# Optimization experiments

Measured on AMD Instinct MI355X. Metric: run time of the kernel, lower is better.

Reference implementation:

```python
import jax, jax.numpy as jnp
import numpy as np

B, N, C = 8192, 4, 4096
SINKHORN_ITERS = 3
EPS = 1e-6


def setup_inputs() -> dict:
    key = jax.random.key(0)
    k_x, k_w, k_pre, k_post, k_res = jax.random.split(key, 5)
    x = jax.random.normal(k_x, (B, N, C), dtype=jnp.float32)
    # Parameters (torch inits: weight=ones, H_pre/H_post=zeros, H_res=eye);
    # use small random perturbations so gradients/normalizations are nontrivial.
    rmsnorm_weight = jnp.ones((C,), jnp.float32) + 0.01 * jax.random.normal(k_w, (C,), jnp.float32)
    H_pre = 0.1 * jax.random.normal(k_pre, (N,), jnp.float32)
    H_post = 0.1 * jax.random.normal(k_post, (N,), jnp.float32)
    H_res = jnp.eye(N, dtype=jnp.float32) + 0.1 * jax.random.normal(k_res, (N, N), jnp.float32)
    return {"x": x, "rmsnorm_weight": rmsnorm_weight, "H_pre": H_pre, "H_post": H_post, "H_res": H_res}


def reference(x, rmsnorm_weight, H_pre, H_post, H_res):
    xf = x.astype(jnp.float32)                                  # [B, n, C]
    # stream aggregation with sigmoid-gated pre-weights
    H_pre_act = jax.nn.sigmoid(H_pre)                           # [n]
    x_agg = jnp.einsum('bnc,n->bc', xf, H_pre_act)              # [B, C]
    # bf16 round-trip mirrors the torch .to(bfloat16) cast before RMSNorm
    x_agg_bf = x_agg.astype(jnp.bfloat16).astype(jnp.float32)
    rms = jnp.sqrt(jnp.mean(x_agg_bf ** 2, axis=-1, keepdims=True) + EPS)  # [B, 1]
    y_norm = x_agg_bf / rms * rmsnorm_weight[None, :]           # [B, C]
    # Sinkhorn-Knopp: doubly-stochastic projection of exp(H_res), n x n (tiny)
    P = jnp.exp(H_res)
    for _ in range(SINKHORN_ITERS):
        P = P / (jnp.sum(P, axis=-1, keepdims=True) + EPS)
        P = P / (jnp.sum(P, axis=-2, keepdims=True) + EPS)
    H_post_act = 2.0 * jax.nn.sigmoid(H_post)                   # [n]
    mixed = jnp.einsum('ij,bjc->bic', P, xf)                    # [B, n, C]
    return mixed + H_post_act[None, :, None] * y_norm[:, None, :]
```

## Files before the change

kernel.cpp:

```cpp
#include <hip/hip_runtime.h>
#include <hip/hip_bf16.h>


constexpr int Bb = 8192;
constexpr int Nn = 4;
constexpr int Cc = 4096;
constexpr int THREADS = 256;
constexpr int C4 = Cc / 4;
constexpr int VPT = C4 / THREADS;

__global__ __launch_bounds__(THREADS)
void mhc_kernel(const float* __restrict__ x,
                const float* __restrict__ w,
                const float* __restrict__ H_pre,
                const float* __restrict__ H_post,
                const float* __restrict__ H_res,
                float* __restrict__ out)
{
    const int b = blockIdx.x;
    const int t = threadIdx.x;

    float pre[4], post[4], P[4][4];
#pragma unroll
    for (int n = 0; n < 4; ++n) {
        pre[n]  = 1.0f / (1.0f + expf(-H_pre[n]));
        post[n] = 2.0f / (1.0f + expf(-H_post[n]));
    }
#pragma unroll
    for (int i = 0; i < 4; ++i)
#pragma unroll
        for (int j = 0; j < 4; ++j)
            P[i][j] = expf(H_res[i * 4 + j]);
#pragma unroll
    for (int it = 0; it < 3; ++it) {
#pragma unroll
        for (int i = 0; i < 4; ++i) {
            float s = P[i][0] + P[i][1] + P[i][2] + P[i][3] + 1e-6f;
            float r = 1.0f / s;
#pragma unroll
            for (int j = 0; j < 4; ++j) P[i][j] *= r;
        }
#pragma unroll
        for (int j = 0; j < 4; ++j) {
            float s = P[0][j] + P[1][j] + P[2][j] + P[3][j] + 1e-6f;
            float r = 1.0f / s;
#pragma unroll
            for (int i = 0; i < 4; ++i) P[i][j] *= r;
        }
    }

    const float4* xb = (const float4*)(x + (size_t)b * Nn * Cc);
    float4 xv[4][VPT];
#pragma unroll
    for (int n = 0; n < 4; ++n)
#pragma unroll
        for (int v = 0; v < VPT; ++v)
            xv[n][v] = xb[n * C4 + v * THREADS + t];

    float4 aggbf[VPT];
    float ssq = 0.0f;
#pragma unroll
    for (int v = 0; v < VPT; ++v) {
        float4 a;
        a.x = pre[0]*xv[0][v].x + pre[1]*xv[1][v].x + pre[2]*xv[2][v].x + pre[3]*xv[3][v].x;
        a.y = pre[0]*xv[0][v].y + pre[1]*xv[1][v].y + pre[2]*xv[2][v].y + pre[3]*xv[3][v].y;
        a.z = pre[0]*xv[0][v].z + pre[1]*xv[1][v].z + pre[2]*xv[2][v].z + pre[3]*xv[3][v].z;
        a.w = pre[0]*xv[0][v].w + pre[1]*xv[1][v].w + pre[2]*xv[2][v].w + pre[3]*xv[3][v].w;
        a.x = __bfloat162float(__float2bfloat16(a.x));
        a.y = __bfloat162float(__float2bfloat16(a.y));
        a.z = __bfloat162float(__float2bfloat16(a.z));
        a.w = __bfloat162float(__float2bfloat16(a.w));
        ssq += a.x*a.x + a.y*a.y + a.z*a.z + a.w*a.w;
        aggbf[v] = a;
    }

#pragma unroll
    for (int off = 32; off > 0; off >>= 1)
        ssq += __shfl_down(ssq, off, 64);
    __shared__ float wsum[4];
    const int wid  = t >> 6;
    const int lane = t & 63;
    if (lane == 0) wsum[wid] = ssq;
    __syncthreads();
    const float tot = wsum[0] + wsum[1] + wsum[2] + wsum[3];
    const float rms_inv = 1.0f / sqrtf(tot * (1.0f / (float)Cc) + 1e-6f);

    const float4* w4 = (const float4*)w;
    float4* ob = (float4*)(out + (size_t)b * Nn * Cc);
#pragma unroll
    for (int v = 0; v < VPT; ++v) {
        const int idx = v * THREADS + t;
        const float4 wv = w4[idx];
        float4 yn;
        yn.x = aggbf[v].x * rms_inv * wv.x;
        yn.y = aggbf[v].y * rms_inv * wv.y;
        yn.z = aggbf[v].z * rms_inv * wv.z;
        yn.w = aggbf[v].w * rms_inv * wv.w;
#pragma unroll
        for (int i = 0; i < 4; ++i) {
            float4 o;
            o.x = P[i][0]*xv[0][v].x + P[i][1]*xv[1][v].x + P[i][2]*xv[2][v].x + P[i][3]*xv[3][v].x + post[i]*yn.x;
            o.y = P[i][0]*xv[0][v].y + P[i][1]*xv[1][v].y + P[i][2]*xv[2][v].y + P[i][3]*xv[3][v].y + post[i]*yn.y;
            o.z = P[i][0]*xv[0][v].z + P[i][1]*xv[1][v].z + P[i][2]*xv[2][v].z + P[i][3]*xv[3][v].z + post[i]*yn.z;
            o.w = P[i][0]*xv[0][v].w + P[i][1]*xv[1][v].w + P[i][2]*xv[2][v].w + P[i][3]*xv[3][v].w + post[i]*yn.w;
            ob[i * C4 + idx] = o;
        }
    }
}

extern "C" void kernel_launch(void* const* d_in, const int* in_sizes, int n_in,
                              void* d_out, int out_size, void* d_ws, size_t ws_size,
                              hipStream_t stream) {
    const float* x      = (const float*)d_in[0];
    const float* w      = (const float*)d_in[1];
    const float* H_pre  = (const float*)d_in[2];
    const float* H_post = (const float*)d_in[3];
    const float* H_res  = (const float*)d_in[4];
    float* out = (float*)d_out;
    mhc_kernel<<<Bb, THREADS, 0, stream>>>(x, w, H_pre, H_post, H_res, out);
}
```

Baseline: 860.2 us.

## Precompute Sinkhorn params in prep kernel and use 1024-thread blocks

Moves the sigmoid and Sinkhorn computation into a tiny one-thread prep kernel that writes 24 parameters to workspace, so the main kernel only loads them instead of recomputing per block. The main kernel now uses 1024 threads per row, each thread handling one float4 column per stream, which cuts per-thread register use from 16 float4 values to 4. The aim is to lower per-block setup cost and raise memory-level parallelism in a bandwidth-bound kernel. It adds a second launch and a 16-wave block reduction with a larger barrier.

```diff
diff --git a/kernel.cpp b/kernel.cpp
--- a/kernel.cpp
+++ b/kernel.cpp
@@ -3,19 +3,43 @@
 
 
 constexpr int Bb = 8192;
-constexpr int Nn = 4;
 constexpr int Cc = 4096;
-constexpr int THREADS = 256;
 constexpr int C4 = Cc / 4;
-constexpr int VPT = C4 / THREADS;
+constexpr int THREADS = 1024;
+
+__global__ __launch_bounds__(64)
+void mhc_prep(const float* __restrict__ H_pre,
+              const float* __restrict__ H_post,
+              const float* __restrict__ H_res,
+              float* __restrict__ prm)
+{
+    if (threadIdx.x != 0) return;
+    float P[4][4];
+    for (int i = 0; i < 4; ++i)
+        for (int j = 0; j < 4; ++j)
+            P[i][j] = expf(H_res[i * 4 + j]);
+    for (int it = 0; it < 3; ++it) {
+        for (int i = 0; i < 4; ++i) {
+            float r = 1.0f / (P[i][0] + P[i][1] + P[i][2] + P[i][3] + 1e-6f);
+            for (int j = 0; j < 4; ++j) P[i][j] *= r;
+        }
+        for (int j = 0; j < 4; ++j) {
+            float r = 1.0f / (P[0][j] + P[1][j] + P[2][j] + P[3][j] + 1e-6f);
+            for (int i = 0; i < 4; ++i) P[i][j] *= r;
+        }
+    }
+    for (int n = 0; n < 4; ++n) {
+        prm[n]     = 1.0f / (1.0f + expf(-H_pre[n]));
+        prm[4 + n] = 2.0f / (1.0f + expf(-H_post[n]));
+    }
+    for (int k = 0; k < 16; ++k) prm[8 + k] = P[k >> 2][k & 3];
+}
 
 __global__ __launch_bounds__(THREADS)
-void mhc_kernel(const float* __restrict__ x,
-                const float* __restrict__ w,
-                const float* __restrict__ H_pre,
-                const float* __restrict__ H_post,
-                const float* __restrict__ H_res,
-                float* __restrict__ out)
+void mhc_main(const float* __restrict__ x,
+              const float* __restrict__ w,
+              const float* __restrict__ prm,
+              float* __restrict__ out)
 {
     const int b = blockIdx.x;
     const int t = threadIdx.x;
@@ -23,88 +47,61 @@
     float pre[4], post[4], P[4][4];
 #pragma unroll
     for (int n = 0; n < 4; ++n) {
-        pre[n]  = 1.0f / (1.0f + expf(-H_pre[n]));
-        post[n] = 2.0f / (1.0f + expf(-H_post[n]));
+        pre[n]  = prm[n];
+        post[n] = prm[4 + n];
     }
 #pragma unroll
     for (int i = 0; i < 4; ++i)
 #pragma unroll
         for (int j = 0; j < 4; ++j)
-            P[i][j] = expf(H_res[i * 4 + j]);
-#pragma unroll
-    for (int it = 0; it < 3; ++it) {
-#pragma unroll
-        for (int i = 0; i < 4; ++i) {
-            float s = P[i][0] + P[i][1] + P[i][2] + P[i][3] + 1e-6f;
-            float r = 1.0f / s;
-#pragma unroll
-            for (int j = 0; j < 4; ++j) P[i][j] *= r;
-        }
-#pragma unroll
-        for (int j = 0; j < 4; ++j) {
-            float s = P[0][j] + P[1][j] + P[2][j] + P[3][j] + 1e-6f;
-            float r = 1.0f / s;
-#pragma unroll
-            for (int i = 0; i < 4; ++i) P[i][j] *= r;
-        }
-    }
+            P[i][j] = prm[8 + i * 4 + j];
 
-    const float4* xb = (const float4*)(x + (size_t)b * Nn * Cc);
-    float4 xv[4][VPT];
-#pragma unroll
-    for (int n = 0; n < 4; ++n)
-#pragma unroll
-        for (int v = 0; v < VPT; ++v)
-            xv[n][v] = xb[n * C4 + v * THREADS + t];
+    const float4* xb = (const float4*)(x + (size_t)b * 4 * Cc);
+    float4 x0 = xb[t];
+    float4 x1 = xb[C4 + t];
+    float4 x2 = xb[2 * C4 + t];
+    float4 x3 = xb[3 * C4 + t];
 
-    float4 aggbf[VPT];
-    float ssq = 0.0f;
-#pragma unroll
-    for (int v = 0; v < VPT; ++v) {
-        float4 a;
-        a.x = pre[0]*xv[0][v].x + pre[1]*xv[1][v].x + pre[2]*xv[2][v].x + pre[3]*xv[3][v].x;
-        a.y = pre[0]*xv[0][v].y + pre[1]*xv[1][v].y + pre[2]*xv[2][v].y + pre[3]*xv[3][v].y;
-        a.z = pre[0]*xv[0][v].z + pre[1]*xv[1][v].z + pre[2]*xv[2][v].z + pre[3]*xv[3][v].z;
-        a.w = pre[0]*xv[0][v].w + pre[1]*xv[1][v].w + pre[2]*xv[2][v].w + pre[3]*xv[3][v].w;
-        a.x = __bfloat162float(__float2bfloat16(a.x));
-        a.y = __bfloat162float(__float2bfloat16(a.y));
-        a.z = __bfloat162float(__float2bfloat16(a.z));
-        a.w = __bfloat162float(__float2bfloat16(a.w));
-        ssq += a.x*a.x + a.y*a.y + a.z*a.z + a.w*a.w;
-        aggbf[v] = a;
-    }
+    float4 a;
+    a.x = pre[0]*x0.x + pre[1]*x1.x + pre[2]*x2.x + pre[3]*x3.x;
+    a.y = pre[0]*x0.y + pre[1]*x1.y + pre[2]*x2.y + pre[3]*x3.y;
+    a.z = pre[0]*x0.z + pre[1]*x1.z + pre[2]*x2.z + pre[3]*x3.z;
+    a.w = pre[0]*x0.w + pre[1]*x1.w + pre[2]*x2.w + pre[3]*x3.w;
+    a.x = __bfloat162float(__float2bfloat16(a.x));
+    a.y = __bfloat162float(__float2bfloat16(a.y));
+    a.z = __bfloat162float(__float2bfloat16(a.z));
+    a.w = __bfloat162float(__float2bfloat16(a.w));
+    float ssq = a.x*a.x + a.y*a.y + a.z*a.z + a.w*a.w;
 
 #pragma unroll
     for (int off = 32; off > 0; off >>= 1)
         ssq += __shfl_down(ssq, off, 64);
-    __shared__ float wsum[4];
+    __shared__ float wsum[16];
     const int wid  = t >> 6;
     const int lane = t & 63;
     if (lane == 0) wsum[wid] = ssq;
     __syncthreads();
-    const float tot = wsum[0] + wsum[1] + wsum[2] + wsum[3];
+    float tot = 0.0f;
+#pragma unroll
+    for (int k = 0; k < 16; ++k) tot += wsum[k];
     const float rms_inv = 1.0f / sqrtf(tot * (1.0f / (float)Cc) + 1e-6f);
 
-    const float4* w4 = (const float4*)w;
-    float4* ob = (float4*)(out + (size_t)b * Nn * Cc);
+    const float4 wv = ((const float4*)w)[t];
+    float4 yn;
+    yn.x = a.x * rms_inv * wv.x;
+    yn.y = a.y * rms_inv * wv.y;
+    yn.z = a.z * rms_inv * wv.z;
+    yn.w = a.w * rms_inv * wv.w;
+
+    float4* ob = (float4*)(out + (size_t)b * 4 * Cc);
 #pragma unroll
-    for (int v = 0; v < VPT; ++v) {
-        const int idx = v * THREADS + t;
-        const float4 wv = w4[idx];
-        float4 yn;
-        yn.x = aggbf[v].x * rms_inv * wv.x;
-        yn.y = aggbf[v].y * rms_inv * wv.y;
-        yn.z = aggbf[v].z * rms_inv * wv.z;
-        yn.w = aggbf[v].w * rms_inv * wv.w;
-#pragma unroll
-        for (int i = 0; i < 4; ++i) {
-            float4 o;
-            o.x = P[i][0]*xv[0][v].x + P[i][1]*xv[1][v].x + P[i][2]*xv[2][v].x + P[i][3]*xv[3][v].x + post[i]*yn.x;
-            o.y = P[i][0]*xv[0][v].y + P[i][1]*xv[1][v].y + P[i][2]*xv[2][v].y + P[i][3]*xv[3][v].y + post[i]*yn.y;
-            o.z = P[i][0]*xv[0][v].z + P[i][1]*xv[1][v].z + P[i][2]*xv[2][v].z + P[i][3]*xv[3][v].z + post[i]*yn.z;
-            o.w = P[i][0]*xv[0][v].w + P[i][1]*xv[1][v].w + P[i][2]*xv[2][v].w + P[i][3]*xv[3][v].w + post[i]*yn.w;
-            ob[i * C4 + idx] = o;
-        }
+    for (int i = 0; i < 4; ++i) {
+        float4 o;
+        o.x = P[i][0]*x0.x + P[i][1]*x1.x + P[i][2]*x2.x + P[i][3]*x3.x + post[i]*yn.x;
+        o.y = P[i][0]*x0.y + P[i][1]*x1.y + P[i][2]*x2.y + P[i][3]*x3.y + post[i]*yn.y;
+        o.z = P[i][0]*x0.z + P[i][1]*x1.z + P[i][2]*x2.z + P[i][3]*x3.z + post[i]*yn.z;
+        o.w = P[i][0]*x0.w + P[i][1]*x1.w + P[i][2]*x2.w + P[i][3]*x3.w + post[i]*yn.w;
+        ob[i * C4 + t] = o;
     }
 }
 
@@ -116,6 +113,9 @@
     const float* H_pre  = (const float*)d_in[2];
     const float* H_post = (const float*)d_in[3];
     const float* H_res  = (const float*)d_in[4];
+    float* prm = (float*)d_ws;
     float* out = (float*)d_out;
-    mhc_kernel<<<Bb, THREADS, 0, stream>>>(x, w, H_pre, H_post, H_res, out);
+
+    mhc_prep<<<1, 64, 0, stream>>>(H_pre, H_post, H_res, prm);
+    mhc_main<<<Bb, THREADS, 0, stream>>>(x, w, prm, out);
 }
```

New measurement: 848.6 us. No clear change (-1.3%).
